# Kernel optimization log

Hardware: AMD Instinct MI355X
Metric: run time of the kernel (lower is better)

The kernel has to match this reference:

```python
import jax, jax.numpy as jnp
import numpy as np

N, E = 50000, 800000
IN, HID, EMB, PROJ = 256, 256, 128, 128


def setup_inputs() -> dict:
    key = jax.random.key(0)
    ks = jax.random.split(key, 10)
    s_in = 1.0 / np.sqrt(IN)
    s_hid = 1.0 / np.sqrt(HID)
    s_emb = 1.0 / np.sqrt(EMB)
    s_proj = 1.0 / np.sqrt(PROJ)
    return {
        "x": jax.random.normal(ks[0], (N, IN), jnp.float32),
        "edge_row": jax.random.randint(ks[1], (E,), 0, N),
        "edge_col": jax.random.randint(ks[2], (E,), 0, N),
        "edge_val": jax.random.uniform(ks[3], (E,), jnp.float32),
        "W1": jax.random.normal(ks[4], (IN, HID), jnp.float32) * s_in,
        "b1": jnp.zeros((HID,), jnp.float32),
        "W2": jax.random.normal(ks[5], (HID, HID), jnp.float32) * s_hid,
        "b2": jnp.zeros((HID,), jnp.float32),
        "W3": jax.random.normal(ks[6], (HID, EMB), jnp.float32) * s_hid,
        "b3": jnp.zeros((EMB,), jnp.float32),
        "P1": jax.random.normal(ks[7], (EMB, PROJ), jnp.float32) * s_emb,
        "pb1": jnp.zeros((PROJ,), jnp.float32),
        "P2": jax.random.normal(ks[8], (PROJ, PROJ), jnp.float32) * s_proj,
        "pb2": jnp.zeros((PROJ,), jnp.float32),
    }


def reference(x, edge_row, edge_col, edge_val, W1, b1, W2, b2, W3, b3, P1, pb1, P2, pb2):
    n = x.shape[0]
    # GCNConv is called as conv(x, Adj.t()): transpose swaps row/col.
    # gcn_norm: add self loops (value 1), symmetric normalization D^-1/2 (A+I) D^-1/2.
    loops = jnp.arange(n)
    r = jnp.concatenate([edge_col, loops])  # adj_t rows (destinations)
    c = jnp.concatenate([edge_row, loops])  # adj_t cols (sources)
    v = jnp.concatenate([edge_val, jnp.ones((n,), x.dtype)])
    deg = jax.ops.segment_sum(v, r, num_segments=n)
    dinv = jnp.where(deg > 0, deg ** -0.5, 0.0).astype(x.dtype)
    nv = dinv[r] * v * dinv[c]  # [E+N] normalized edge weights

    def agg(h):  # spmm: out[i] = sum_e nv[e] * h[c[e]] scattered to r[e]
        return jax.ops.segment_sum(nv[:, None] * h[c], r, num_segments=n)

    h = jax.nn.relu(agg(x @ W1) + b1)      # dropout is identity in eval
    h = jax.nn.relu(agg(h @ W2) + b2)
    emb = agg(h @ W3) + b3
    z = jax.nn.relu(emb @ P1 + pb1) @ P2 + pb2
    return emb, z
```

## Files before the change

kernel.cpp:

```cpp
#include <hip/hip_runtime.h>
#include <hip/hip_bf16.h>
#include <cstdint>
#include <cstddef>

#define NN 50000
#define NE 800000
#define NRBP 3128
#define NBK 196
#define BKCAP 4608

typedef __attribute__((ext_vector_type(8))) short bf16x8;
typedef __attribute__((ext_vector_type(4))) float f32x4;

#define OUT_BF16ROW 0
#define OUT_FRAG    1
#define OUT_F32     2

static __device__ __forceinline__ unsigned short f2bf_u(float f) {
    __hip_bfloat16 h = __float2bfloat16(f);
    return *reinterpret_cast<unsigned short*>(&h);
}
static __device__ __forceinline__ float bfu2f(unsigned short u) {
    __hip_bfloat16 h = *reinterpret_cast<__hip_bfloat16*>(&u);
    return __bfloat162float(h);
}

static __device__ __forceinline__ void gll16(void* lds_dst, const void* gsrc) {
    __builtin_amdgcn_global_load_lds(
        (const __attribute__((address_space(1))) void*)gsrc,
        (__attribute__((address_space(3))) void*)lds_dst, 16, 0, 0);
}


__global__ __launch_bounds__(256) void k_bscat(const int* __restrict__ erow,
                                               const int* __restrict__ ecol,
                                               const float* __restrict__ eval_,
                                               int* __restrict__ gcur,
                                               int2* __restrict__ tmp, int e) {
    __shared__ int lcnt[NBK], lbase[NBK], lcur[NBK];
    int tid = threadIdx.x;
    for (int t = tid; t < NBK; t += 256) { lcnt[t] = 0; lcur[t] = 0; }
    __syncthreads();
    int d_[4], b_[4];
#pragma unroll
    for (int q = 0; q < 4; ++q) {
        int i = blockIdx.x * 1024 + q * 256 + tid;
        d_[q] = -1;
        if (i < e) {
            d_[q] = ecol[i];
            b_[q] = d_[q] >> 8;
            atomicAdd(&lcnt[b_[q]], 1);
        }
    }
    __syncthreads();
    for (int t = tid; t < NBK; t += 256)
        lbase[t] = lcnt[t] ? (t * BKCAP + atomicAdd(&gcur[t], lcnt[t])) : 0;
    __syncthreads();
#pragma unroll
    for (int q = 0; q < 4; ++q) {
        int i = blockIdx.x * 1024 + q * 256 + tid;
        if (i < e) {
            int b = b_[q];
            int pos = lbase[b] + atomicAdd(&lcur[b], 1);
            tmp[pos] = make_int2(erow[i] | ((d_[q] & 255) << 20), __float_as_int(eval_[i]));
        }
    }
}

__global__ __launch_bounds__(256) void k_bsort(const int2* __restrict__ tmp,
                                               const int* __restrict__ cnt,
                                               int2* __restrict__ rowrange,
                                               float* __restrict__ dinv,
                                               int2* __restrict__ epk) {
    __shared__ int lcnt[256], lcur[256];
    __shared__ float ldeg[256];
    __shared__ int wsum[4];
    int tid = threadIdx.x;
    int b = blockIdx.x;
    int base = b * BKCAP, endb = base + cnt[b];
    lcnt[tid] = 0;
    ldeg[tid] = 0.f;
    __syncthreads();
    for (int i = base + tid; i < endb; i += 256) {
        int2 e2 = tmp[i];
        int d = e2.x >> 20;
        atomicAdd(&lcnt[d], 1);
        atomicAdd(&ldeg[d], __int_as_float(e2.y));
    }
    __syncthreads();
    int v = lcnt[tid];
    int lane = tid & 63, w = tid >> 6;
    int incl = v;
#pragma unroll
    for (int d = 1; d < 64; d <<= 1) {
        int t = __shfl_up(incl, d);
        if (lane >= d) incl += t;
    }
    if (lane == 63) wsum[w] = incl;
    __syncthreads();
    int woff = 0;
    for (int j = 0; j < w; ++j) woff += wsum[j];
    int ex = woff + incl - v;
    int dest = (b << 8) + tid;
    if (dest < NN) {
        rowrange[dest] = make_int2(base + ex, base + ex + v);
        dinv[dest] = rsqrtf(1.f + ldeg[tid]);
    }
    lcur[tid] = ex;
    __syncthreads();
    for (int i = base + tid; i < endb; i += 256) {
        int2 e2 = tmp[i];
        int d = e2.x >> 20;
        int pos = base + atomicAdd(&lcur[d], 1);
        epk[pos] = make_int2(e2.x & 0xFFFFF, e2.y);
    }
}

__global__ void k_normw(int2* __restrict__ epk, const float* __restrict__ dinv,
                        const int* __restrict__ cnt) {
    int i = blockIdx.x * 256 + threadIdx.x;
    if (i >= NBK * BKCAP) return;
    int b = i / BKCAP;
    if (i - b * BKCAP < cnt[b]) {
        int2 pk = epk[i];
        epk[i].y = __float_as_int(__int_as_float(pk.y) * dinv[pk.x]);
    }
}

template<int DIM, bool RELU, int OMODE>
__global__ __launch_bounds__(256) void k_agg(const unsigned short* __restrict__ H,
                      const int2* __restrict__ rowrange, const int2* __restrict__ epk,
                      const float* __restrict__ dinv, const float* __restrict__ bias,
                      float* __restrict__ outf, unsigned short* __restrict__ oh) {
    constexpr int WU = DIM / 128;
    int lane = threadIdx.x & 63;
    int row = blockIdx.x * 4 + (threadIdx.x >> 6);
    if (row >= NN) return;

    const uint2* H2 = reinterpret_cast<const uint2*>(H);
    const unsigned* H1 = reinterpret_cast<const unsigned*>(H);

    auto loadrow = [&](int r, unsigned* v) {
        if constexpr (WU == 2) {
            uint2 t = H2[(size_t)r * 64 + lane];
            v[0] = t.x; v[1] = t.y;
        } else {
            v[0] = H1[(size_t)r * 64 + lane];
        }
    };

    float di = dinv[row];
    float acc[WU * 2];
    {
        unsigned sv[WU];
        loadrow(row, sv);
#pragma unroll
        for (int w2 = 0; w2 < WU; ++w2) {
            acc[w2 * 2 + 0] = di * __uint_as_float(sv[w2] << 16);
            acc[w2 * 2 + 1] = di * __uint_as_float(sv[w2] & 0xffff0000u);
        }
    }

    auto accum = [&](const unsigned* v, float wt) {
#pragma unroll
        for (int w2 = 0; w2 < WU; ++w2) {
            acc[w2 * 2 + 0] += wt * __uint_as_float(v[w2] << 16);
            acc[w2 * 2 + 1] += wt * __uint_as_float(v[w2] & 0xffff0000u);
        }
    };

    int2 rr = rowrange[row];
    int beg = rr.x, end = rr.y;
    for (int c = beg; c < end; c += 64) {
        int m = min(64, end - c);
        int2 pk = make_int2(0, 0);
        if (c + lane < end) pk = epk[c + lane];
        int j = 0;
        for (; j + 8 <= m; j += 8) {
            int s[8];
            float wv[8];
#pragma unroll
            for (int q = 0; q < 8; ++q) {
                s[q] = __shfl(pk.x, j + q);
                wv[q] = __int_as_float(__shfl(pk.y, j + q));
            }
            unsigned g[8][WU];
#pragma unroll
            for (int q = 0; q < 8; ++q) loadrow(s[q], g[q]);
#pragma unroll
            for (int q = 0; q < 8; ++q) accum(g[q], wv[q]);
        }
        for (; j < m; ++j) {
            int s = __shfl(pk.x, j);
            float wt = __int_as_float(__shfl(pk.y, j));
            unsigned g[WU];
            loadrow(s, g);
            accum(g, wt);
        }
    }

    if constexpr (OMODE == 1) {
        float4 b4 = reinterpret_cast<const float4*>(bias)[lane];
        float o0 = acc[0] * di + b4.x;
        float o1 = acc[1] * di + b4.y;
        float o2 = acc[2] * di + b4.z;
        float o3 = acc[3] * di + b4.w;
        if (RELU) {
            o0 = fmaxf(o0, 0.f); o1 = fmaxf(o1, 0.f);
            o2 = fmaxf(o2, 0.f); o3 = fmaxf(o3, 0.f);
        }
        ushort4 h;
        h.x = f2bf_u(o0); h.y = f2bf_u(o1); h.z = f2bf_u(o2); h.w = f2bf_u(o3);
        size_t ch = (size_t)(lane >> 3) * NRBP + (row >> 4);
        int off = ((lane & 7) >> 1) * 128 + (row & 15) * 8 + (lane & 1) * 4;
        *reinterpret_cast<ushort4*>(&oh[ch * 512 + off]) = h;
    } else if constexpr (WU == 2) {
        float4 b4 = reinterpret_cast<const float4*>(bias)[lane];
        float4 o;
        o.x = acc[0] * di + b4.x; o.y = acc[1] * di + b4.y;
        o.z = acc[2] * di + b4.z; o.w = acc[3] * di + b4.w;
        if (RELU) {
            o.x = fmaxf(o.x, 0.f); o.y = fmaxf(o.y, 0.f);
            o.z = fmaxf(o.z, 0.f); o.w = fmaxf(o.w, 0.f);
        }
        reinterpret_cast<float4*>(outf)[(size_t)row * 64 + lane] = o;
    } else {
        float2 b2 = reinterpret_cast<const float2*>(bias)[lane];
        float o0 = acc[0] * di + b2.x;
        float o1 = acc[1] * di + b2.y;
        if (RELU) { o0 = fmaxf(o0, 0.f); o1 = fmaxf(o1, 0.f); }
        reinterpret_cast<float2*>(outf)[(size_t)row * 64 + lane] = make_float2(o0, o1);
        if constexpr (OMODE == 2) {
            int c0 = 2 * lane;
            int kb = c0 >> 5, kg = (c0 & 31) >> 3, kj = c0 & 7;
            size_t ch = (size_t)kb * NRBP + (row >> 4);
            int off = kg * 128 + (row & 15) * 8 + kj;
            ushort2 h2s;
            h2s.x = f2bf_u(o0); h2s.y = f2bf_u(o1);
            *reinterpret_cast<ushort2*>(&oh[ch * 512 + off]) = h2s;
        }
    }
}

__global__ void k_xsplit(const float* __restrict__ X, unsigned short* __restrict__ xh,
                         int nrows) {
    int idx = blockIdx.x * 256 + threadIdx.x;
    int row = idx >> 6, t = idx & 63;
    if (row >= nrows) return;
    float4 v = *reinterpret_cast<const float4*>(&X[(size_t)row * 256 + t * 4]);
    ushort4 h;
    h.x = f2bf_u(v.x); h.y = f2bf_u(v.y); h.z = f2bf_u(v.z); h.w = f2bf_u(v.w);
    size_t chunk = (size_t)(t >> 3) * NRBP + (row >> 4);
    int off = ((t & 7) >> 1) * 128 + (row & 15) * 8 + (t & 1) * 4;
    *reinterpret_cast<ushort4*>(&xh[chunk * 512 + off]) = h;
}

__global__ void k_wsplit(const float* __restrict__ W, unsigned short* __restrict__ wh,
                         unsigned short* __restrict__ wl, int K, int M) {
    int idx = blockIdx.x * blockDim.x + threadIdx.x;
    if (idx >= K * M) return;
    int k = idx / M, m = idx % M;
    float w = W[idx];
    unsigned short h = f2bf_u(w);
    float hf = bfu2f(h);
    unsigned short lo = f2bf_u(w - hf);
    int kb = k >> 5, kg = (k & 31) >> 3, kj = k & 7;
    int nb = m >> 4, c = m & 15;
    int off = (kb * (M >> 4) + nb) * 512 + kg * 128 + c * 8 + kj;
    wh[off] = h;
    wl[off] = lo;
}

template<int BM, int BN, int OMODE, bool RELU>
__global__ __launch_bounds__((BM / 64) * (BN / 64) * 64)
void k_mmf(const unsigned short* __restrict__ ah,
           const unsigned short* __restrict__ wh, const unsigned short* __restrict__ wl,
           const float* __restrict__ bias, void* __restrict__ Cout,
           int nrows, int K, int M) {
    constexpr int NW = (BM / 64) * (BN / 64);
    constexpr int WN = BN / 64;
    constexpr int AC = BM / 16, BC = BN / 16;
    constexpr int TC = AC + 2 * BC;
    constexpr int BUF = TC * 512;
    __shared__ unsigned short sm[2 * BUF];
    const int tid = threadIdx.x, l = tid & 63, wid = tid >> 6;
    const int wr = wid / WN, wc = wid % WN;
    const int bm = blockIdx.x * BM, bn = blockIdx.y * BN;
    const int rb0 = blockIdx.x * AC, nb0 = blockIdx.y * BC;
    const int NKB = K >> 5, MB = M >> 4;
    const int fo = (l >> 4) * 128 + (l & 15) * 8;
    f32x4 acc[4][4] = {};

    auto stage = [&](int buf, int kb) {
        unsigned short* base = sm + buf * BUF;
        const unsigned short* ga_h = ah + ((size_t)kb * NRBP + rb0) * 512;
        const unsigned short* gb_h = wh + ((size_t)kb * MB + nb0) * 512;
        const unsigned short* gb_l = wl + ((size_t)kb * MB + nb0) * 512;
        for (int q = wid; q < TC; q += NW) {
            const unsigned short* s;
            if (q < AC) s = ga_h + q * 512;
            else if (q < AC + BC) s = gb_h + (q - AC) * 512;
            else s = gb_l + (q - AC - BC) * 512;
            gll16(base + q * 512, s + l * 8);
        }
    };

    stage(0, 0);
    __syncthreads();
    for (int kb = 0; kb < NKB; ++kb) {
        const int cur = kb & 1;
        if (kb + 1 < NKB) stage(cur ^ 1, kb + 1);
        const unsigned short* base = sm + cur * BUF;
        bf16x8 a_h[4], b_h[4], b_l[4];
#pragma unroll
        for (int i = 0; i < 4; ++i)
            a_h[i] = *reinterpret_cast<const bf16x8*>(base + (wr * 4 + i) * 512 + fo);
#pragma unroll
        for (int j = 0; j < 4; ++j) {
            b_h[j] = *reinterpret_cast<const bf16x8*>(base + (AC + wc * 4 + j) * 512 + fo);
            b_l[j] = *reinterpret_cast<const bf16x8*>(base + (AC + BC + wc * 4 + j) * 512 + fo);
        }
#pragma unroll
        for (int i = 0; i < 4; ++i)
#pragma unroll
            for (int j = 0; j < 4; ++j) {
                acc[i][j] = __builtin_amdgcn_mfma_f32_16x16x32_bf16(a_h[i], b_h[j], acc[i][j], 0, 0, 0);
                acc[i][j] = __builtin_amdgcn_mfma_f32_16x16x32_bf16(a_h[i], b_l[j], acc[i][j], 0, 0, 0);
            }
        __syncthreads();
    }
#pragma unroll
    for (int j = 0; j < 4; ++j) {
        int col = bn + wc * 64 + j * 16 + (l & 15);
        float bv = (OMODE != OUT_BF16ROW) ? bias[col] : 0.f;
#pragma unroll
        for (int i = 0; i < 4; ++i) {
            int row0 = bm + wr * 64 + i * 16 + (l >> 4) * 4;
#pragma unroll
            for (int r = 0; r < 4; ++r) {
                int row = row0 + r;
                if (row >= nrows) continue;
                float v = acc[i][j][r] + bv;
                if (RELU) v = fmaxf(v, 0.f);
                if constexpr (OMODE == OUT_BF16ROW) {
                    ((unsigned short*)Cout)[(size_t)row * M + col] = f2bf_u(v);
                } else if constexpr (OMODE == OUT_FRAG) {
                    size_t ch = (size_t)(col >> 5) * NRBP + (row >> 4);
                    int off = ((col & 31) >> 3) * 128 + (row & 15) * 8 + (col & 7);
                    ((unsigned short*)Cout)[ch * 512 + off] = f2bf_u(v);
                } else {
                    ((float*)Cout)[(size_t)row * M + col] = v;
                }
            }
        }
    }
}


extern "C" void kernel_launch(void* const* d_in, const int* in_sizes, int n_in,
                              void* d_out, int out_size, void* d_ws, size_t ws_size,
                              hipStream_t stream) {
    const float* x        = (const float*)d_in[0];
    const int*   edge_row = (const int*)d_in[1];
    const int*   edge_col = (const int*)d_in[2];
    const float* edge_val = (const float*)d_in[3];
    const float* W1  = (const float*)d_in[4];
    const float* b1  = (const float*)d_in[5];
    const float* W2  = (const float*)d_in[6];
    const float* b2  = (const float*)d_in[7];
    const float* W3  = (const float*)d_in[8];
    const float* b3  = (const float*)d_in[9];
    const float* P1  = (const float*)d_in[10];
    const float* pb1 = (const float*)d_in[11];
    const float* P2  = (const float*)d_in[12];
    const float* pb2 = (const float*)d_in[13];

    const int N = NN, E = NE;
    const size_t EPAD = (size_t)NBK * BKCAP;

    uintptr_t p = (uintptr_t)d_ws;
    auto alloc = [&](size_t bytes) -> void* {
        void* r = (void*)p;
        p += (bytes + 255) & ~(size_t)255;
        return r;
    };
    float* dinv     = (float*)alloc((size_t)N * 4);
    int2*  rowrange = (int2*)alloc((size_t)N * 8);
    int*   gcur     = (int*)alloc(256 * 4);
    int2*  etmp     = (int2*)alloc(EPAD * 8);
    int2*  epk      = (int2*)alloc(EPAD * 8);
    unsigned short* Hbf = (unsigned short*)alloc((size_t)N * 256 * 2);
    const size_t PLANE8 = (size_t)8 * NRBP * 512 * 2;
    const size_t PLANE4 = (size_t)4 * NRBP * 512 * 2;
    unsigned short* pAh   = (unsigned short*)alloc(PLANE8);
    unsigned short* pBh   = (unsigned short*)alloc(PLANE8);
    unsigned short* embF  = (unsigned short*)alloc(PLANE4);
    unsigned short* bufTF = (unsigned short*)alloc(PLANE4);
    unsigned short* wf1h = (unsigned short*)alloc(65536 * 2);
    unsigned short* wf1l = (unsigned short*)alloc(65536 * 2);
    unsigned short* wf2h = (unsigned short*)alloc(65536 * 2);
    unsigned short* wf2l = (unsigned short*)alloc(65536 * 2);
    unsigned short* wf3h = (unsigned short*)alloc(32768 * 2);
    unsigned short* wf3l = (unsigned short*)alloc(32768 * 2);
    unsigned short* p1h  = (unsigned short*)alloc(16384 * 2);
    unsigned short* p1l  = (unsigned short*)alloc(16384 * 2);
    unsigned short* p2h  = (unsigned short*)alloc(16384 * 2);
    unsigned short* p2l  = (unsigned short*)alloc(16384 * 2);

    float* emb = (float*)d_out;
    float* z   = (float*)d_out + (size_t)N * 128;

    dim3 b256(256);
    const int gE1k = (E + 1023) / 1024;

    k_wsplit<<<dim3(256), b256, 0, stream>>>(W1, wf1h, wf1l, 256, 256);
    k_wsplit<<<dim3(256), b256, 0, stream>>>(W2, wf2h, wf2l, 256, 256);
    k_wsplit<<<dim3(128), b256, 0, stream>>>(W3, wf3h, wf3l, 256, 128);
    k_wsplit<<<dim3(64),  b256, 0, stream>>>(P1, p1h, p1l, 128, 128);
    k_wsplit<<<dim3(64),  b256, 0, stream>>>(P2, p2h, p2l, 128, 128);
    k_xsplit<<<dim3((N * 64 + 255) / 256), b256, 0, stream>>>(x, pAh, N);

    hipMemsetAsync(gcur, 0, 256 * 4, stream);
    k_bscat<<<dim3(gE1k), b256, 0, stream>>>(edge_row, edge_col, edge_val, gcur, etmp, E);
    k_bsort<<<dim3(NBK), b256, 0, stream>>>(etmp, gcur, rowrange, dinv, epk);
    k_normw<<<dim3((int)((EPAD + 255) / 256)), b256, 0, stream>>>(epk, dinv, gcur);

    const int gagg = (N + 3) / 4;

    k_mmf<128, 128, OUT_BF16ROW, false><<<dim3(391, 2), dim3(256), 0, stream>>>(
        pAh, wf1h, wf1l, nullptr, Hbf, N, 256, 256);
    k_agg<256, true, 1><<<dim3(gagg), b256, 0, stream>>>(Hbf, rowrange, epk, dinv, b1, nullptr, pBh);
    k_mmf<128, 128, OUT_BF16ROW, false><<<dim3(391, 2), dim3(256), 0, stream>>>(
        pBh, wf2h, wf2l, nullptr, Hbf, N, 256, 256);
    k_agg<256, true, 1><<<dim3(gagg), b256, 0, stream>>>(Hbf, rowrange, epk, dinv, b2, nullptr, pAh);
    k_mmf<64, 128, OUT_BF16ROW, false><<<dim3(782, 1), dim3(128), 0, stream>>>(
        pAh, wf3h, wf3l, nullptr, Hbf, N, 256, 128);
    k_agg<128, false, 2><<<dim3(gagg), b256, 0, stream>>>(Hbf, rowrange, epk, dinv, b3, emb, embF);
    k_mmf<64, 128, OUT_FRAG, true><<<dim3(782, 1), dim3(128), 0, stream>>>(
        embF, p1h, p1l, pb1, bufTF, N, 128, 128);
    k_mmf<64, 128, OUT_F32, false><<<dim3(782, 1), dim3(128), 0, stream>>>(
        bufTF, p2h, p2l, pb2, z, N, 128, 128);
}
```

Before: 346.6 us.

## Merge input prep kernels into one launch and shrink aggregation unroll

```diff
diff --git a/kernel.cpp b/kernel.cpp
--- a/kernel.cpp
+++ b/kernel.cpp
@@ -29,6 +29,56 @@
     __builtin_amdgcn_global_load_lds(
         (const __attribute__((address_space(1))) void*)gsrc,
         (__attribute__((address_space(3))) void*)lds_dst, 16, 0, 0);
+}
+
+__global__ __launch_bounds__(256) void k_prep(
+        const float* __restrict__ X,
+        const float* __restrict__ W1, const float* __restrict__ W2,
+        const float* __restrict__ W3, const float* __restrict__ P1,
+        const float* __restrict__ P2,
+        unsigned short* __restrict__ xh,
+        unsigned short* __restrict__ w1h, unsigned short* __restrict__ w1l,
+        unsigned short* __restrict__ w2h, unsigned short* __restrict__ w2l,
+        unsigned short* __restrict__ w3h, unsigned short* __restrict__ w3l,
+        unsigned short* __restrict__ p1h, unsigned short* __restrict__ p1l,
+        unsigned short* __restrict__ p2h, unsigned short* __restrict__ p2l,
+        int* __restrict__ gcur) {
+    int b = blockIdx.x;
+    int tid = threadIdx.x;
+    if (b < 12500) {
+        int idx = b * 256 + tid;
+        int row = idx >> 6, t = idx & 63;
+        if (row < NN) {
+            float4 v = *reinterpret_cast<const float4*>(&X[(size_t)row * 256 + t * 4]);
+            ushort4 h;
+            h.x = f2bf_u(v.x); h.y = f2bf_u(v.y); h.z = f2bf_u(v.z); h.w = f2bf_u(v.w);
+            size_t chunk = (size_t)(t >> 3) * NRBP + (row >> 4);
+            int off = ((t & 7) >> 1) * 128 + (row & 15) * 8 + (t & 1) * 4;
+            *reinterpret_cast<ushort4*>(&xh[chunk * 512 + off]) = h;
+        }
+        return;
+    }
+    int wb = b - 12500;
+    if (wb == 0) gcur[tid] = 0;
+    const float* W;
+    unsigned short *wh, *wl;
+    int K, M;
+    if (wb < 256)      { W = W1; wh = w1h; wl = w1l; K = 256; M = 256; }
+    else if (wb < 512) { W = W2; wh = w2h; wl = w2l; K = 256; M = 256; wb -= 256; }
+    else if (wb < 640) { W = W3; wh = w3h; wl = w3l; K = 256; M = 128; wb -= 512; }
+    else if (wb < 704) { W = P1; wh = p1h; wl = p1l; K = 128; M = 128; wb -= 640; }
+    else               { W = P2; wh = p2h; wl = p2l; K = 128; M = 128; wb -= 704; }
+    int idx = wb * 256 + tid;
+    if (idx >= K * M) return;
+    int k = idx / M, m = idx % M;
+    float w = W[idx];
+    unsigned short h = f2bf_u(w);
+    unsigned short lo = f2bf_u(w - bfu2f(h));
+    int kb = k >> 5, kg = (k & 31) >> 3, kj = k & 7;
+    int nb = m >> 4, c = m & 15;
+    int off = (kb * (M >> 4) + nb) * 512 + kg * 128 + c * 8 + kj;
+    wh[off] = h;
+    wl[off] = lo;
 }
 
 
@@ -176,19 +226,22 @@
         int2 pk = make_int2(0, 0);
         if (c + lane < end) pk = epk[c + lane];
         int j = 0;
-        for (; j + 8 <= m; j += 8) {
-            int s[8];
-            float wv[8];
-#pragma unroll
-            for (int q = 0; q < 8; ++q) {
-                s[q] = __shfl(pk.x, j + q);
-                wv[q] = __int_as_float(__shfl(pk.y, j + q));
-            }
-            unsigned g[8][WU];
-#pragma unroll
-            for (int q = 0; q < 8; ++q) loadrow(s[q], g[q]);
-#pragma unroll
-            for (int q = 0; q < 8; ++q) accum(g[q], wv[q]);
+        for (; j + 4 <= m; j += 4) {
+            int s0 = __shfl(pk.x, j + 0), s1 = __shfl(pk.x, j + 1);
+            int s2 = __shfl(pk.x, j + 2), s3 = __shfl(pk.x, j + 3);
+            float w0 = __int_as_float(__shfl(pk.y, j + 0));
+            float w1 = __int_as_float(__shfl(pk.y, j + 1));
+            float w2 = __int_as_float(__shfl(pk.y, j + 2));
+            float w3 = __int_as_float(__shfl(pk.y, j + 3));
+            unsigned g0[WU], g1[WU], g2[WU], g3[WU];
+            loadrow(s0, g0);
+            loadrow(s1, g1);
+            loadrow(s2, g2);
+            loadrow(s3, g3);
+            accum(g0, w0);
+            accum(g1, w1);
+            accum(g2, w2);
+            accum(g3, w3);
         }
         for (; j < m; ++j) {
             int s = __shfl(pk.x, j);
@@ -240,35 +293,6 @@
             *reinterpret_cast<ushort2*>(&oh[ch * 512 + off]) = h2s;
         }
     }
-}
-
-__global__ void k_xsplit(const float* __restrict__ X, unsigned short* __restrict__ xh,
-                         int nrows) {
-    int idx = blockIdx.x * 256 + threadIdx.x;
-    int row = idx >> 6, t = idx & 63;
-    if (row >= nrows) return;
-    float4 v = *reinterpret_cast<const float4*>(&X[(size_t)row * 256 + t * 4]);
-    ushort4 h;
-    h.x = f2bf_u(v.x); h.y = f2bf_u(v.y); h.z = f2bf_u(v.z); h.w = f2bf_u(v.w);
-    size_t chunk = (size_t)(t >> 3) * NRBP + (row >> 4);
-    int off = ((t & 7) >> 1) * 128 + (row & 15) * 8 + (t & 1) * 4;
-    *reinterpret_cast<ushort4*>(&xh[chunk * 512 + off]) = h;
-}
-
-__global__ void k_wsplit(const float* __restrict__ W, unsigned short* __restrict__ wh,
-                         unsigned short* __restrict__ wl, int K, int M) {
-    int idx = blockIdx.x * blockDim.x + threadIdx.x;
-    if (idx >= K * M) return;
-    int k = idx / M, m = idx % M;
-    float w = W[idx];
-    unsigned short h = f2bf_u(w);
-    float hf = bfu2f(h);
-    unsigned short lo = f2bf_u(w - hf);
-    int kb = k >> 5, kg = (k & 31) >> 3, kj = k & 7;
-    int nb = m >> 4, c = m & 15;
-    int off = (kb * (M >> 4) + nb) * 512 + kg * 128 + c * 8 + kj;
-    wh[off] = h;
-    wl[off] = lo;
 }
 
 template<int BM, int BN, int OMODE, bool RELU>
@@ -413,14 +437,10 @@
     dim3 b256(256);
     const int gE1k = (E + 1023) / 1024;
 
-    k_wsplit<<<dim3(256), b256, 0, stream>>>(W1, wf1h, wf1l, 256, 256);
-    k_wsplit<<<dim3(256), b256, 0, stream>>>(W2, wf2h, wf2l, 256, 256);
-    k_wsplit<<<dim3(128), b256, 0, stream>>>(W3, wf3h, wf3l, 256, 128);
-    k_wsplit<<<dim3(64),  b256, 0, stream>>>(P1, p1h, p1l, 128, 128);
-    k_wsplit<<<dim3(64),  b256, 0, stream>>>(P2, p2h, p2l, 128, 128);
-    k_xsplit<<<dim3((N * 64 + 255) / 256), b256, 0, stream>>>(x, pAh, N);
-
-    hipMemsetAsync(gcur, 0, 256 * 4, stream);
+    k_prep<<<dim3(12500 + 768), b256, 0, stream>>>(
+        x, W1, W2, W3, P1, P2, pAh,
+        wf1h, wf1l, wf2h, wf2l, wf3h, wf3l, p1h, p1l, p2h, p2l, gcur);
+
     k_bscat<<<dim3(gE1k), b256, 0, stream>>>(edge_row, edge_col, edge_val, gcur, etmp, E);
     k_bsort<<<dim3(NBK), b256, 0, stream>>>(etmp, gcur, rowrange, dinv, epk);
     k_normw<<<dim3((int)((EPAD + 255) / 256)), b256, 0, stream>>>(epk, dinv, gcur);
```

Result: faster. 329.5 us (-5.0%).
